# Optimization experiments

Hardware: AMD Instinct MI355X
Metric: run time of the kernel (lower is better)

## Reference

```python
import jax, jax.numpy as jnp
import numpy as np
import math

B, T, N, IN_FEAT = 2, 64, 128, 2
H_LSTM = IN_FEAT * 2   # 4
D = IN_FEAT * 4        # 8
FH, FW = 16, 16
C_MAP = 2048
C_COMP = 32
TH = 0.5
IMG = 512.0


def setup_inputs() -> dict:
    key = jax.random.key(0)
    ks = jax.random.split(key, 20)
    s = 0.02
    inp = {
        "x": jax.random.uniform(ks[0], (B, 2, T, N), jnp.float32) * IMG,  # pixel coords in [0,512)
        "metadata": jax.random.normal(ks[1], (B, C_MAP, FH, FW), jnp.float32),
        # LSTM(in_feat, 2*in_feat): gates order i,f,g,o
        "w_ih": jax.random.normal(ks[2], (4 * H_LSTM, IN_FEAT), jnp.float32) * s,
        "w_hh": jax.random.normal(ks[3], (4 * H_LSTM, H_LSTM), jnp.float32) * s,
        "b_ih": jax.random.normal(ks[4], (4 * H_LSTM,), jnp.float32) * s,
        "b_hh": jax.random.normal(ks[5], (4 * H_LSTM,), jnp.float32) * s,
        "fc_w": jax.random.normal(ks[6], (D, H_LSTM), jnp.float32) * s,
        "fc_b": jax.random.normal(ks[7], (D,), jnp.float32) * s,
        "fc2_w": jax.random.normal(ks[8], (D, IN_FEAT), jnp.float32) * s,
        "fc2_b": jax.random.normal(ks[9], (D,), jnp.float32) * s,
        "fc3_w": jax.random.normal(ks[10], (D, IN_FEAT), jnp.float32) * s,
        "fc3_b": jax.random.normal(ks[11], (D,), jnp.float32) * s,
        "comp_w": jax.random.normal(ks[12], (C_COMP, C_MAP), jnp.float32) * s,
        "comp_b": jax.random.normal(ks[13], (C_COMP,), jnp.float32) * s,
        "vf_w": jax.random.normal(ks[14], (H_LSTM, H_LSTM + C_COMP), jnp.float32) * s,
        "vf_b": jax.random.normal(ks[15], (H_LSTM,), jnp.float32) * s,
        "fcout_w": jax.random.normal(ks[16], (IN_FEAT, D), jnp.float32) * s,
        "fcout_b": jax.random.normal(ks[17], (IN_FEAT,), jnp.float32) * s,
    }
    return inp


def _grid_sample_bilinear(fm, grid):
    # fm: [B,C,H,W]; grid: [B,P,1,2] normalized (x,y) in [-1,1]; bilinear, zeros padding, align_corners=False
    Bb, C, Hh, Ww = fm.shape
    gx, gy = grid[..., 0], grid[..., 1]              # [B,P,1]
    ix = ((gx + 1.0) * Ww - 1.0) * 0.5
    iy = ((gy + 1.0) * Hh - 1.0) * 0.5
    ix0 = jnp.floor(ix); iy0 = jnp.floor(iy)
    wx = ix - ix0; wy = iy - iy0

    def gather(f, yy, xx):
        valid = ((yy >= 0) & (yy < Hh) & (xx >= 0) & (xx < Ww)).astype(f.dtype)
        yc = jnp.clip(yy, 0, Hh - 1).astype(jnp.int32)
        xc = jnp.clip(xx, 0, Ww - 1).astype(jnp.int32)
        return f[:, yc, xc] * valid[None]            # [C,P,1]

    def per_batch(f, x0, y0, wx_, wy_):
        x1 = x0 + 1.0; y1 = y0 + 1.0
        return (gather(f, y0, x0) * ((1 - wy_) * (1 - wx_))[None]
                + gather(f, y0, x1) * ((1 - wy_) * wx_)[None]
                + gather(f, y1, x0) * (wy_ * (1 - wx_))[None]
                + gather(f, y1, x1) * (wy_ * wx_)[None])

    return jax.vmap(per_batch)(fm, ix0, iy0, wx, wy)  # [B,C,P,1]


def reference(x, metadata, w_ih, w_hh, b_ih, b_hh, fc_w, fc_b, fc2_w, fc2_b,
              fc3_w, fc3_b, comp_w, comp_b, vf_w, vf_b, fcout_w, fcout_b):
    coords = x                                        # [B,2,T,N] raw pixel coords
    xp = jnp.transpose(x, (0, 2, 3, 1))               # [B,T,N,2]
    b, t, n, c = xp.shape

    # sinusoidal positional encoding over time axis
    div = jnp.exp(jnp.arange(0, c, 2, dtype=jnp.float32) * (-math.log(10000.0) / c))
    pos = jnp.arange(t, dtype=jnp.float32)[:, None]
    pe = jnp.zeros((t, c), xp.dtype)
    pe = pe.at[:, 0::2].set(jnp.sin(pos * div))
    pe = pe.at[:, 1::2].set(jnp.cos(pos * div))
    xp = xp + pe[None, :, None, :]
    xr = xp.reshape(-1, c)                            # [M,2], M=b*t*n

    # single-step LSTM with zero init state (seq_len==1 in original)
    gates = xr @ w_ih.T + b_ih + b_hh                 # h0=0 => W_hh term vanishes
    i, f, g, o = jnp.split(gates, 4, axis=-1)
    cst = jax.nn.sigmoid(i) * jnp.tanh(g)
    X = jax.nn.sigmoid(o) * jnp.tanh(cst)             # [M,4]

    # visual fusion: 1x1 conv compressor + grid_sample local context
    comp = jnp.einsum('bchw,oc->bohw', metadata, comp_w) + comp_b[None, :, None, None]
    cgrid = jnp.transpose(coords, (0, 2, 3, 1)).reshape(b, -1, 1, 2)
    ngrid = 2.0 * (cgrid / IMG) - 1.0
    sampled = _grid_sample_bilinear(comp, ngrid)      # [B,32,TN,1]
    lc = jnp.transpose(sampled[..., 0], (0, 2, 1)).reshape(-1, C_COMP)  # [M,32]
    X = jnp.concatenate([X, lc], axis=-1) @ vf_w.T + vf_b               # [M,4]

    # sigmoid-gated full attention over all t*n tokens
    Q = (X @ fc_w.T + fc_b).reshape(b, t * n, -1)     # [B,TN,8]
    K = (xr @ fc2_w.T + fc2_b).reshape(b, t * n, -1)
    V = (xr @ fc3_w.T + fc3_b).reshape(b, t * n, -1)
    probs = jax.nn.sigmoid(jnp.einsum('bqd,bkd->bqk', Q, K))  # [B,TN,TN]
    out = jnp.einsum('bqk,bkd->bqd', probs, V).reshape(-1, Q.shape[-1])

    out = out * (out > TH).astype(out.dtype)          # threshold-ReLU
    out = out @ fcout_w.T + fcout_b                   # [M,2]
    out = out.reshape(b, t, n, -1)
    return jnp.transpose(out, (0, 3, 1, 2))           # [B,2,T,N]
```

## Files before the change

### kernel.cpp

```cpp
#include <hip/hip_runtime.h>
#include <math.h>

#define BB    2
#define TT    64
#define NN    128
#define TN    8192
#define MM    16384
#define CMAP  2048
#define CCOMP 32
#define FHW   256

#define CSPLIT 64
#define CRANGE 32

#define DEG    17
#define NS     18
#define NODD   9
#define MDIM   19
#define NMOMF  (MDIM*MDIM)
#define MCH    64
#define MPTS   128
#define ZFIT   5.0
#define ZFITF  5.0f
#define UVBOUND 1.0045f

struct QCoef { float cb[NS][NODD]; };

#define OFF_CP    0
#define OFF_COMP  (OFF_CP + CSPLIT*BB*FHW*CCOMP)
#define OFF_X     (OFF_COMP + BB*FHW*CCOMP)
#define OFF_MP    (OFF_X + MM*2)
#define OFF_MF    (OFF_MP + BB*MCH*NMOMF)

__device__ __forceinline__ float fast_sigmoid(float v) {
    return __builtin_amdgcn_rcpf(1.0f + __expf(-v));
}
__device__ __forceinline__ float fast_tanh(float v) {
    return 1.0f - 2.0f * __builtin_amdgcn_rcpf(1.0f + __expf(2.0f * v));
}

__global__ void __launch_bounds__(256) k_pre(const float* __restrict__ x,
                                             const float* __restrict__ metadata,
                                             const float* __restrict__ comp_w,
                                             float* __restrict__ Cp,
                                             float2* __restrict__ Xr,
                                             float* __restrict__ Mp) {
    __shared__ float lds[2 * MPTS * MDIM];

    const int blk = blockIdx.x;
    const int tid = threadIdx.x;

    if (blk < 128) {
        const int b  = blk & 1;
        const int cs = blk >> 1;
        float (*wcs)[CCOMP] = (float(*)[CCOMP])lds;
        for (int i = tid; i < CRANGE * CCOMP; i += 256) {
            int c = i >> 5, o = i & 31;
            wcs[c][o] = comp_w[o * CMAP + cs * CRANGE + c];
        }
        __syncthreads();

        float acc[CCOMP];
#pragma unroll
        for (int o = 0; o < CCOMP; o++) acc[o] = 0.0f;

        const float* mb = metadata + ((size_t)b * CMAP + (size_t)cs * CRANGE) * FHW + tid;
#pragma unroll 4
        for (int c = 0; c < CRANGE; c++) {
            float mv = mb[c * FHW];
#pragma unroll
            for (int o = 0; o < CCOMP; o++) acc[o] += mv * wcs[c][o];
        }

        float* outp = Cp + (size_t)cs * (BB * FHW * CCOMP) + ((size_t)b * FHW + tid) * CCOMP;
#pragma unroll
        for (int o = 0; o < CCOMP; o += 4)
            *(float4*)&outp[o] = make_float4(acc[o], acc[o + 1], acc[o + 2], acc[o + 3]);
    } else {
        const int idx = blk - 128;
        const int b  = idx & 1;
        const int ch = idx >> 1;
        float (*spu)[MDIM] = (float(*)[MDIM])lds;
        float (*spv)[MDIM] = (float(*)[MDIM])(lds + MPTS * MDIM);

        if (tid < MPTS) {
            const int p = ch * MPTS + tid;
            const int t = p >> 7;
            const float px = x[(size_t)(b * 2 + 0) * TN + p];
            const float py = x[(size_t)(b * 2 + 1) * TN + p];
            const float xr0 = px + __sinf((float)t);
            const float xr1 = py + __cosf((float)t);
            Xr[b * TN + p] = make_float2(xr0, xr1);

            const float u = (xr0 - 256.0f) * (1.0f / 256.0f);
            const float v = (xr1 - 256.0f) * (1.0f / 256.0f);
            float a = 1.0f, c = 1.0f;
#pragma unroll
            for (int i = 0; i < MDIM; i++) {
                spu[tid][i] = a; spv[tid][i] = c;
                a *= u; c *= v;
            }
        }
        __syncthreads();

        float* outp = Mp + ((size_t)(b * MCH + ch)) * NMOMF;
        for (int i = tid; i < NMOMF; i += 256) {
            const int j = i / MDIM, l = i % MDIM;
            float s = 0.0f;
            if (j + l < MDIM) {
#pragma unroll 8
                for (int p = 0; p < MPTS; p++)
                    s += spu[p][j] * spv[p][l];
            }
            outp[i] = s;
        }
    }
}

__global__ void __launch_bounds__(256) k_reduce(const float* __restrict__ Cp,
                                                const float* __restrict__ comp_b,
                                                float* __restrict__ comp_ws,
                                                const float* __restrict__ Mp,
                                                float* __restrict__ Mf) {
    const int blk = blockIdx.x;
    const int tid = threadIdx.x;

    if (blk < 64) {
        const int i = blk * 256 + tid;
        float s = 0.0f;
#pragma unroll 16
        for (int cs = 0; cs < CSPLIT; cs++)
            s += Cp[(size_t)cs * (BB * FHW * CCOMP) + i];
        comp_ws[i] = s + comp_b[i & (CCOMP - 1)];
    } else {
        const int gi = (blk - 64) * 256 + tid;
        if (gi < BB * NMOMF) {
            const int b = gi / NMOMF;
            const int i = gi - b * NMOMF;
            float s = 0.0f;
#pragma unroll 16
            for (int ch = 0; ch < MCH; ch++)
                s += Mp[((size_t)(b * MCH + ch)) * NMOMF + i];
            Mf[gi] = s;
        }
    }
}

__global__ void __launch_bounds__(256) k_main(
        const float* __restrict__ x,
        const float* __restrict__ w_ih,
        const float* __restrict__ b_ih,  const float* __restrict__ b_hh,
        const float* __restrict__ fc_w,  const float* __restrict__ fc_b,
        const float* __restrict__ fc2_w, const float* __restrict__ fc2_b,
        const float* __restrict__ fc3_w, const float* __restrict__ fc3_b,
        const float* __restrict__ vf_w,  const float* __restrict__ vf_b,
        const float* __restrict__ fcout_w, const float* __restrict__ fcout_b,
        const float* __restrict__ comp_ws,
        const float2* __restrict__ Xr,
        const float* __restrict__ Mf,
        float* __restrict__ y, QCoef qc) {
    __shared__ float sM[NMOMF];

    const int tid = threadIdx.x;
    const int m   = blockIdx.x * 256 + tid;
    const int b   = m >> 13;
    const int p   = m & (TN - 1);
    const int t   = p >> 7;

    for (int i = tid; i < NMOMF; i += 256) sM[i] = Mf[b * NMOMF + i];

    const float px = x[(size_t)(b * 2 + 0) * TN + p];
    const float py = x[(size_t)(b * 2 + 1) * TN + p];
    const float xr0 = px + __sinf((float)t);
    const float xr1 = py + __cosf((float)t);

    float X[4];
#pragma unroll
    for (int j = 0; j < 4; j++) {
        float gi = xr0 * w_ih[(j)      * 2] + xr1 * w_ih[(j)      * 2 + 1] + b_ih[j]      + b_hh[j];
        float gg = xr0 * w_ih[(8 + j)  * 2] + xr1 * w_ih[(8 + j)  * 2 + 1] + b_ih[8 + j]  + b_hh[8 + j];
        float go = xr0 * w_ih[(12 + j) * 2] + xr1 * w_ih[(12 + j) * 2 + 1] + b_ih[12 + j] + b_hh[12 + j];
        float cst = fast_sigmoid(gi) * fast_tanh(gg);
        X[j] = fast_sigmoid(go) * fast_tanh(cst);
    }

    float lc[CCOMP];
#pragma unroll
    for (int c = 0; c < CCOMP; c++) lc[c] = 0.0f;

    const float ix = px * (1.0f / 32.0f) - 0.5f;
    const float iy = py * (1.0f / 32.0f) - 0.5f;
    const float fx0 = floorf(ix), fy0 = floorf(iy);
    const float wx = ix - fx0, wy = iy - fy0;
    const int x0 = (int)fx0, y0 = (int)fy0;
    const float* cb = comp_ws + (size_t)b * FHW * CCOMP;

#pragma unroll
    for (int dy = 0; dy < 2; dy++) {
#pragma unroll
        for (int dx = 0; dx < 2; dx++) {
            int xx = x0 + dx, yy = y0 + dy;
            if (xx < 0 || xx > 15 || yy < 0 || yy > 15) continue;
            float w = (dy ? wy : 1.0f - wy) * (dx ? wx : 1.0f - wx);
            const float4* cp4 = (const float4*)(cb + (yy * 16 + xx) * CCOMP);
#pragma unroll
            for (int c4 = 0; c4 < CCOMP / 4; c4++) {
                float4 v = cp4[c4];
                lc[c4 * 4 + 0] += w * v.x;
                lc[c4 * 4 + 1] += w * v.y;
                lc[c4 * 4 + 2] += w * v.z;
                lc[c4 * 4 + 3] += w * v.w;
            }
        }
    }

    float X2[4];
#pragma unroll
    for (int j = 0; j < 4; j++) {
        float a = vf_b[j];
#pragma unroll
        for (int k = 0; k < 4; k++) a += X[k] * vf_w[j * 36 + k];
#pragma unroll
        for (int c = 0; c < CCOMP; c++) a += lc[c] * vf_w[j * 36 + 4 + c];
        X2[j] = a;
    }

    float al = 0.0f, be = 0.0f, ga = 0.0f;
#pragma unroll
    for (int d = 0; d < 8; d++) {
        float q = fc_b[d];
#pragma unroll
        for (int k = 0; k < 4; k++) q += X2[k] * fc_w[d * 4 + k];
        al += q * fc2_b[d];
        be += q * fc2_w[d * 2];
        ga += q * fc2_w[d * 2 + 1];
    }

    __syncthreads();

    const float b1 = 256.0f * be;
    const float c1 = 256.0f * ga;
    const float a0 = al + 256.0f * (be + ga);

    float S0, S1, S2;
    const float zb = fabsf(a0) + UVBOUND * (fabsf(b1) + fabsf(c1));
    if (zb >= ZFITF) {
        float s0 = 0.0f, s1 = 0.0f, s2 = 0.0f;
        const float2* xp = Xr + b * TN;
        for (int k = 0; k < TN; k++) {
            float2 kv = xp[k];
            float z = al + be * kv.x + ga * kv.y;
            float sg = fast_sigmoid(z);
            s0 += sg; s1 += sg * kv.x; s2 += sg * kv.y;
        }
        S0 = s0; S1 = s1; S2 = s2;
    } else {
        float pa[NS];
        pa[0] = 1.0f;
#pragma unroll
        for (int tt = 1; tt < NS; tt++) pa[tt] = pa[tt - 1] * a0;

        float A[NS];
#pragma unroll
        for (int s = 0; s < NS; s++) {
            float acc = 0.0f;
            const int t0 = (s & 1) ? 0 : 1;
#pragma unroll
            for (int q = 0; q < NODD; q++) {
                const int tt = t0 + 2 * q;
                if (s + tt <= DEG) acc = fmaf(qc.cb[s][q], pa[tt], acc);
            }
            A[s] = acc;
        }

        float R0 = A[0] * sM[0];
        float R1 = A[0] * sM[1 * MDIM + 0];
        float R2 = A[0] * sM[0 * MDIM + 1];

        float Ep[NS], Ec[NS];
        Ep[0] = 1.0f;
#pragma unroll
        for (int s = 1; s < NS; s++) {
            Ec[0] = c1 * Ep[0];
#pragma unroll
            for (int j = 1; j < NS; j++)
                if (j < s) Ec[j] = fmaf(b1, Ep[j - 1], c1 * Ep[j]);
            Ec[s] = b1 * Ep[s - 1];

            float W = 0.0f, W1 = 0.0f, W2 = 0.0f;
#pragma unroll
            for (int j = 0; j < NS; j++) {
                if (j <= s) {
                    const int l = s - j;
                    const float e = Ec[j];
                    W  = fmaf(e, sM[j * MDIM + l],       W);
                    W1 = fmaf(e, sM[(j + 1) * MDIM + l], W1);
                    W2 = fmaf(e, sM[j * MDIM + l + 1],   W2);
                }
            }
            R0 = fmaf(A[s], W,  R0);
            R1 = fmaf(A[s], W1, R1);
            R2 = fmaf(A[s], W2, R2);
#pragma unroll
            for (int j = 0; j < NS; j++)
                if (j <= s) Ep[j] = Ec[j];
        }

        S0 = 4096.0f + R0;
        const float su = 0.5f * sM[1 * MDIM + 0] + R1;
        const float sv = 0.5f * sM[0 * MDIM + 1] + R2;
        S1 = 256.0f * su + 256.0f * S0;
        S2 = 256.0f * sv + 256.0f * S0;
    }

    float f0 = fcout_b[0], f1 = fcout_b[1];
#pragma unroll
    for (int d = 0; d < 8; d++) {
        float vv = S0 * fc3_b[d] + S1 * fc3_w[d * 2] + S2 * fc3_w[d * 2 + 1];
        vv = (vv > 0.5f) ? vv : 0.0f;
        f0 += vv * fcout_w[d];
        f1 += vv * fcout_w[8 + d];
    }
    y[(size_t)(b * 2 + 0) * TN + p] = f0;
    y[(size_t)(b * 2 + 1) * TN + p] = f1;
}

static QCoef compute_qcoef() {
    const int NNODE = 64;
    const double PI = 3.14159265358979323846;
    double term[NODD];
    for (int i = 0; i < NODD; ++i) term[i] = 0.0;

    for (int jn = 0; jn < NNODE; ++jn) {
        double theta = (jn + 0.5) * (PI / NNODE);
        double ct = cos(theta);
        double zj = ZFIT * ct;
        double fj = 1.0 / (1.0 + exp(-zj)) - 0.5;
        double Ckm2 = 1.0, Ckm1 = ct;
        term[0] += fj * ct;
        int idx = 1;
        for (int k = 2; k <= DEG; ++k) {
            double Ck = 2.0 * ct * Ckm1 - Ckm2;
            Ckm2 = Ckm1; Ckm1 = Ck;
            if (k & 1) term[idx++] += fj * Ck;
        }
    }

    double c[DEG + 1];
    for (int i = 0; i <= DEG; ++i) c[i] = 0.0;
    for (int i = 0; i < NODD; ++i) c[2 * i + 1] = term[i] * (2.0 / NNODE);

    double Tm2[DEG + 1], Tm1[DEG + 1], a[DEG + 1];
    for (int i = 0; i <= DEG; ++i) { Tm2[i] = 0.0; Tm1[i] = 0.0; a[i] = 0.0; }
    Tm2[0] = 1.0; Tm1[1] = 1.0;
    a[1] = c[1];
    for (int k = 2; k <= DEG; ++k) {
        double Tc[DEG + 1];
        for (int mm = 0; mm <= DEG; ++mm) Tc[mm] = 0.0;
        for (int mm = 0; mm <= k; ++mm) {
            double vv = -Tm2[mm];
            if (mm > 0) vv += 2.0 * Tm1[mm - 1];
            Tc[mm] = vv;
        }
        if (k & 1)
            for (int mm = 1; mm <= k; mm += 2) a[mm] += c[k] * Tc[mm];
        for (int mm = 0; mm <= DEG; ++mm) { Tm2[mm] = Tm1[mm]; Tm1[mm] = Tc[mm]; }
    }

    double Cz[DEG + 1];
    double sc = 1.0;
    for (int mm = 0; mm <= DEG; ++mm) { Cz[mm] = a[mm] * sc; sc *= (1.0 / ZFIT); }

    double Bi[NS][NS];
    for (int n = 0; n < NS; ++n)
        for (int k = 0; k < NS; ++k) Bi[n][k] = 0.0;
    for (int n = 0; n < NS; ++n) {
        Bi[n][0] = 1.0;
        for (int k = 1; k <= n; ++k)
            Bi[n][k] = Bi[n - 1][k - 1] + ((k <= n - 1) ? Bi[n - 1][k] : 0.0);
    }

    QCoef qc;
    for (int s = 0; s < NS; ++s)
        for (int q = 0; q < NODD; ++q) qc.cb[s][q] = 0.0f;
    for (int s = 0; s < NS; ++s) {
        int q = 0;
        for (int t = (s & 1) ? 0 : 1; s + t <= DEG; t += 2)
            qc.cb[s][q++] = (float)(Cz[s + t] * Bi[s + t][s]);
    }
    return qc;
}

extern "C" void kernel_launch(void* const* d_in, const int* in_sizes, int n_in,
                              void* d_out, int out_size, void* d_ws, size_t ws_size,
                              hipStream_t stream) {
    const float* x        = (const float*)d_in[0];
    const float* metadata = (const float*)d_in[1];
    const float* w_ih     = (const float*)d_in[2];
    const float* b_ih     = (const float*)d_in[4];
    const float* b_hh     = (const float*)d_in[5];
    const float* fc_w     = (const float*)d_in[6];
    const float* fc_b     = (const float*)d_in[7];
    const float* fc2_w    = (const float*)d_in[8];
    const float* fc2_b    = (const float*)d_in[9];
    const float* fc3_w    = (const float*)d_in[10];
    const float* fc3_b    = (const float*)d_in[11];
    const float* comp_w   = (const float*)d_in[12];
    const float* comp_b   = (const float*)d_in[13];
    const float* vf_w     = (const float*)d_in[14];
    const float* vf_b     = (const float*)d_in[15];
    const float* fcout_w  = (const float*)d_in[16];
    const float* fcout_b  = (const float*)d_in[17];

    static const QCoef qc = compute_qcoef();

    float*  ws      = (float*)d_ws;
    float*  Cp      = ws + OFF_CP;
    float*  comp_ws = ws + OFF_COMP;
    float2* Xr      = (float2*)(ws + OFF_X);
    float*  Mp      = ws + OFF_MP;
    float*  Mf      = ws + OFF_MF;

    k_pre<<<256, 256, 0, stream>>>(x, metadata, comp_w, Cp, Xr, Mp);

    k_reduce<<<68, 256, 0, stream>>>(Cp, comp_b, comp_ws, Mp, Mf);

    k_main<<<64, 256, 0, stream>>>(x, w_ih, b_ih, b_hh,
                                   fc_w, fc_b, fc2_w, fc2_b,
                                   fc3_w, fc3_b, vf_w, vf_b,
                                   fcout_w, fcout_b,
                                   comp_ws, Xr, Mf, (float*)d_out, qc);
}
```

Baseline: 113.7 us.

## Fold partial-sum reduction into main kernel and drop the reduce launch

Removes the separate k_reduce kernel. Each k_main block now sums the compressor partials and the moment partials for its batch straight into LDS, using a padded stride of 36 so the bilinear gathers read from shared memory instead of global. The channel split is halved (32 splits of 64 channels), which cuts the size of the partial buffer and the number of k_pre blocks. In exchange, every one of the 64 main blocks repeats the same reduction over about 1 MB of partials, which adds L2 traffic and a startup delay before the main work in each block.

```diff
diff --git a/kernel.cpp b/kernel.cpp
--- a/kernel.cpp
+++ b/kernel.cpp
@@ -10,8 +10,8 @@
 #define CCOMP 32
 #define FHW   256
 
-#define CSPLIT 64
-#define CRANGE 32
+#define CSPLIT 32
+#define CRANGE 64
 
 #define DEG    17
 #define NS     18
@@ -24,13 +24,13 @@
 #define ZFITF  5.0f
 #define UVBOUND 1.0045f
 
+#define CSTR   36
+
 struct QCoef { float cb[NS][NODD]; };
 
 #define OFF_CP    0
-#define OFF_COMP  (OFF_CP + CSPLIT*BB*FHW*CCOMP)
-#define OFF_X     (OFF_COMP + BB*FHW*CCOMP)
+#define OFF_X     (OFF_CP + CSPLIT*BB*FHW*CCOMP)
 #define OFF_MP    (OFF_X + MM*2)
-#define OFF_MF    (OFF_MP + BB*MCH*NMOMF)
 
 __device__ __forceinline__ float fast_sigmoid(float v) {
     return __builtin_amdgcn_rcpf(1.0f + __expf(-v));
@@ -50,7 +50,7 @@
     const int blk = blockIdx.x;
     const int tid = threadIdx.x;
 
-    if (blk < 128) {
+    if (blk < 64) {
         const int b  = blk & 1;
         const int cs = blk >> 1;
         float (*wcs)[CCOMP] = (float(*)[CCOMP])lds;
@@ -77,7 +77,7 @@
         for (int o = 0; o < CCOMP; o += 4)
             *(float4*)&outp[o] = make_float4(acc[o], acc[o + 1], acc[o + 2], acc[o + 3]);
     } else {
-        const int idx = blk - 128;
+        const int idx = blk - 64;
         const int b  = idx & 1;
         const int ch = idx >> 1;
         float (*spu)[MDIM] = (float(*)[MDIM])lds;
@@ -117,35 +117,6 @@
     }
 }
 
-__global__ void __launch_bounds__(256) k_reduce(const float* __restrict__ Cp,
-                                                const float* __restrict__ comp_b,
-                                                float* __restrict__ comp_ws,
-                                                const float* __restrict__ Mp,
-                                                float* __restrict__ Mf) {
-    const int blk = blockIdx.x;
-    const int tid = threadIdx.x;
-
-    if (blk < 64) {
-        const int i = blk * 256 + tid;
-        float s = 0.0f;
-#pragma unroll 16
-        for (int cs = 0; cs < CSPLIT; cs++)
-            s += Cp[(size_t)cs * (BB * FHW * CCOMP) + i];
-        comp_ws[i] = s + comp_b[i & (CCOMP - 1)];
-    } else {
-        const int gi = (blk - 64) * 256 + tid;
-        if (gi < BB * NMOMF) {
-            const int b = gi / NMOMF;
-            const int i = gi - b * NMOMF;
-            float s = 0.0f;
-#pragma unroll 16
-            for (int ch = 0; ch < MCH; ch++)
-                s += Mp[((size_t)(b * MCH + ch)) * NMOMF + i];
-            Mf[gi] = s;
-        }
-    }
-}
-
 __global__ void __launch_bounds__(256) k_main(
         const float* __restrict__ x,
         const float* __restrict__ w_ih,
@@ -155,10 +126,12 @@
         const float* __restrict__ fc3_w, const float* __restrict__ fc3_b,
         const float* __restrict__ vf_w,  const float* __restrict__ vf_b,
         const float* __restrict__ fcout_w, const float* __restrict__ fcout_b,
-        const float* __restrict__ comp_ws,
+        const float* __restrict__ comp_b,
+        const float* __restrict__ Cp,
         const float2* __restrict__ Xr,
-        const float* __restrict__ Mf,
+        const float* __restrict__ Mp,
         float* __restrict__ y, QCoef qc) {
+    __shared__ float scomp[FHW * CSTR];
     __shared__ float sM[NMOMF];
 
     const int tid = threadIdx.x;
@@ -167,7 +140,22 @@
     const int p   = m & (TN - 1);
     const int t   = p >> 7;
 
-    for (int i = tid; i < NMOMF; i += 256) sM[i] = Mf[b * NMOMF + i];
+    for (int i = tid; i < FHW * CCOMP; i += 256) {
+        float s = 0.0f;
+#pragma unroll 8
+        for (int cs = 0; cs < CSPLIT; cs++)
+            s += Cp[(size_t)cs * (BB * FHW * CCOMP) + (size_t)b * FHW * CCOMP + i];
+        const int hw = i >> 5, o = i & 31;
+        scomp[hw * CSTR + o] = s + comp_b[o];
+    }
+    for (int i = tid; i < NMOMF; i += 256) {
+        float s = 0.0f;
+#pragma unroll 16
+        for (int ch = 0; ch < MCH; ch++)
+            s += Mp[((size_t)(b * MCH + ch)) * NMOMF + i];
+        sM[i] = s;
+    }
+    __syncthreads();
 
     const float px = x[(size_t)(b * 2 + 0) * TN + p];
     const float py = x[(size_t)(b * 2 + 1) * TN + p];
@@ -193,7 +181,6 @@
     const float fx0 = floorf(ix), fy0 = floorf(iy);
     const float wx = ix - fx0, wy = iy - fy0;
     const int x0 = (int)fx0, y0 = (int)fy0;
-    const float* cb = comp_ws + (size_t)b * FHW * CCOMP;
 
 #pragma unroll
     for (int dy = 0; dy < 2; dy++) {
@@ -202,7 +189,7 @@
             int xx = x0 + dx, yy = y0 + dy;
             if (xx < 0 || xx > 15 || yy < 0 || yy > 15) continue;
             float w = (dy ? wy : 1.0f - wy) * (dx ? wx : 1.0f - wx);
-            const float4* cp4 = (const float4*)(cb + (yy * 16 + xx) * CCOMP);
+            const float4* cp4 = (const float4*)(scomp + (yy * 16 + xx) * CSTR);
 #pragma unroll
             for (int c4 = 0; c4 < CCOMP / 4; c4++) {
                 float4 v = cp4[c4];
@@ -235,8 +222,6 @@
         be += q * fc2_w[d * 2];
         ga += q * fc2_w[d * 2 + 1];
     }
-
-    __syncthreads();
 
     const float b1 = 256.0f * be;
     const float c1 = 256.0f * ga;
@@ -414,20 +399,16 @@
 
     static const QCoef qc = compute_qcoef();
 
-    float*  ws      = (float*)d_ws;
-    float*  Cp      = ws + OFF_CP;
-    float*  comp_ws = ws + OFF_COMP;
-    float2* Xr      = (float2*)(ws + OFF_X);
-    float*  Mp      = ws + OFF_MP;
-    float*  Mf      = ws + OFF_MF;
-
-    k_pre<<<256, 256, 0, stream>>>(x, metadata, comp_w, Cp, Xr, Mp);
-
-    k_reduce<<<68, 256, 0, stream>>>(Cp, comp_b, comp_ws, Mp, Mf);
+    float*  ws = (float*)d_ws;
+    float*  Cp = ws + OFF_CP;
+    float2* Xr = (float2*)(ws + OFF_X);
+    float*  Mp = ws + OFF_MP;
+
+    k_pre<<<192, 256, 0, stream>>>(x, metadata, comp_w, Cp, Xr, Mp);
 
     k_main<<<64, 256, 0, stream>>>(x, w_ih, b_ih, b_hh,
                                    fc_w, fc_b, fc2_w, fc2_b,
                                    fc3_w, fc3_b, vf_w, vf_b,
                                    fcout_w, fcout_b,
-                                   comp_ws, Xr, Mf, (float*)d_out, qc);
-}
+                                   comp_b, Cp, Xr, Mp, (float*)d_out, qc);
+}
```

New measurement: 161.1 us. 41.6% more time.
